# Optimization experiments

Hardware: AMD Instinct MI355X
Metric: run time of the kernel (lower is better)

## Reference

```python
import jax, jax.numpy as jnp
import numpy as np

EPS = 1e-6
B, N, I, H, O, L = 8, 2048, 64, 128, 8, 3
K = O * L
ITERS, TAU, LAM, KNN = 3, 0.1, 0.5, 5

def _ln(x, g, b):
    m = x.mean(-1, keepdims=True)
    v = jnp.mean((x - m) ** 2, -1, keepdims=True)
    return (x - m) / jnp.sqrt(v + 1e-5) * g + b

def _gelu(x):
    return jax.nn.gelu(x, approximate=False)


def setup_inputs():
    ks = jax.random.split(jax.random.key(0), 16)
    rn = lambda k, sh, s=0.05: jax.random.normal(k, sh, jnp.float32) * s
    return {
        'x': jax.random.normal(ks[0], (B, N, I), jnp.float32),
        'enc_w1': rn(ks[1], (H, I)), 'enc_b1': jnp.zeros((H,), jnp.float32),
        'enc_g1': jnp.ones((H,), jnp.float32), 'enc_bb1': jnp.zeros((H,), jnp.float32),
        'enc_w2': rn(ks[2], (H, H)), 'enc_b2': jnp.zeros((H,), jnp.float32),
        'enc_g2': jnp.ones((H,), jnp.float32), 'enc_bb2': jnp.zeros((H,), jnp.float32),
        'sp_w1': rn(ks[3], (H, H + 1)), 'sp_b1': jnp.zeros((H,), jnp.float32),
        'sp_g': jnp.ones((H,), jnp.float32), 'sp_bb': jnp.zeros((H,), jnp.float32),
        'sp_w2': rn(ks[4], (1, H), 0.005), 'sp_b2': jnp.zeros((1,), jnp.float32),
        'object_space': rn(ks[5], (1, O, H), 0.1),
        'horizon_scale': jnp.float32(0.3),
        'level_times': jnp.array([1.0, 2.5, 4.0], jnp.float32),
        'base_horizons': jnp.array([0.9, 0.6, 0.3], jnp.float32),
        'gru_w_ih': rn(ks[6], (3 * H, H)), 'gru_w_hh': rn(ks[7], (3 * H, H)),
        'gru_b_ih': jnp.zeros((3 * H,), jnp.float32), 'gru_b_hh': jnp.zeros((3 * H,), jnp.float32),
        'mlp_w1': rn(ks[8], (H, H)), 'mlp_b1': jnp.zeros((H,), jnp.float32),
        'mlp_w2': rn(ks[9], (H, H)), 'mlp_b2': jnp.zeros((H,), jnp.float32),
        'norm_g': jnp.ones((H,), jnp.float32), 'norm_b': jnp.zeros((H,), jnp.float32),
    }


def reference(x, enc_w1, enc_b1, enc_g1, enc_bb1, enc_w2, enc_b2, enc_g2, enc_bb2, sp_w1, sp_b1, sp_g, sp_bb, sp_w2, sp_b2, object_space, horizon_scale, level_times, base_horizons, gru_w_ih, gru_w_hh, gru_b_ih, gru_b_hh, mlp_w1, mlp_b1, mlp_w2, mlp_b2, norm_g, norm_b):
    # feature encoder: Linear -> LN -> GELU -> Linear -> LN
    h = _gelu(_ln(x @ enc_w1.T + enc_b1, enc_g1, enc_bb1))
    spatial = _ln(h @ enc_w2.T + enc_b2, enc_g2, enc_bb2)  # (B,N,H)
    # local density via kNN mean distance (torch.cdist equivalent)
    sq = jnp.sum(x * x, -1)
    d2 = sq[:, :, None] + sq[:, None, :] - 2.0 * jnp.einsum('bnd,bmd->bnm', x, x)
    dist = jnp.sqrt(jnp.maximum(d2, 0.0))
    knn = -jax.lax.top_k(-dist, KNN + 1)[0]           # k+1 smallest, ascending
    density = jnp.tanh(knn[..., 1:].mean(-1))          # (B,N)
    # scale predictor: Linear -> LN -> GELU -> Linear -> Softplus
    s = jnp.concatenate([spatial, density[..., None]], -1)
    s = _gelu(_ln(s @ sp_w1.T + sp_b1, sp_g, sp_bb))
    pred_scale = jax.nn.softplus(s @ sp_w2.T + sp_b2)  # (B,N,1)
    pred_time = 5.0 - 1.5 * density[..., None] + 0.5 * pred_scale
    features = jnp.concatenate([pred_time, spatial], -1)  # (B,N,H+1)
    # scale-adaptive horizons, tiled object-major to match slot layout
    hz = jnp.clip(base_horizons[None, :, None] + (horizon_scale * (density - 0.5))[:, None, :], 0.1, 1.0)
    horizons = jnp.tile(hz, (1, O, 1))                 # (B,K,N)
    # worldlines
    obj = jnp.broadcast_to(object_space, (B, O, H))
    times = jnp.broadcast_to(jnp.tile(level_times, O)[None, :, None], (B, K, 1))
    slots = jnp.concatenate([times, jnp.repeat(obj, L, axis=1)], -1)  # (B,K,H+1)
    feats_sp = features[..., 1:]
    old_flat = obj.reshape(-1, H)
    attn = None
    for _ in range(ITERS):
        diff = features[:, None, :, :] - slots[:, :, None, :]  # (B,K,N,H+1)
        dt = diff[..., 0]
        dr2 = jnp.sum(diff[..., 1:] ** 2, -1)
        ls = dt * dt - dr2
        d_L = jnp.sign(ls) * jnp.sqrt(jnp.abs(ls) + EPS)
        r = jnp.sqrt(dr2)
        cone = horizons - r / (jnp.abs(dt) + EPS) - 10.0 * jax.nn.relu(-dt) - 5.0 * jax.nn.relu(r - jnp.abs(dt))
        logits = -jnp.abs(d_L) + LAM * jnp.tanh(cone)
        attn = jax.nn.softmax(logits / TAU, axis=1)      # softmax over slots
        w = attn / (attn.sum(2, keepdims=True) + 1e-8)
        upd = jnp.einsum('bkn,bnh->bkh', w, feats_sp)
        obj_upd = upd.reshape(B, O, L, H).sum(2).reshape(-1, H)
        # GRUCell (torch semantics)
        gi = obj_upd @ gru_w_ih.T + gru_b_ih
        gh = old_flat @ gru_w_hh.T + gru_b_hh
        gi_r, gi_z, gi_n = jnp.split(gi, 3, -1)
        gh_r, gh_z, gh_n = jnp.split(gh, 3, -1)
        rg = jax.nn.sigmoid(gi_r + gh_r)
        zg = jax.nn.sigmoid(gi_z + gh_z)
        ng = jnp.tanh(gi_n + rg * gh_n)
        new = ((1.0 - zg) * ng + zg * old_flat).reshape(B, O, H)
        t = _gelu(_ln(new, norm_g, norm_b) @ mlp_w1.T + mlp_b1) @ mlp_w2.T + mlp_b2
        new = new + 0.2 * t
        slots = jnp.concatenate([times, jnp.repeat(new, L, axis=1)], -1)
    return slots, attn, pred_time[..., 0], density
```

## Files before the change

### kernel.cpp

```cpp
#include <hip/hip_runtime.h>
#include <math.h>

constexpr int cB = 8, cN = 2048, cI = 64, cH = 128, cO = 8, cK = 24;
constexpr int ROWS = cB * cN;

constexpr size_t WS_SPATIAL = 0;
constexpr size_t WS_SQ      = WS_SPATIAL + (size_t)ROWS * cH;
constexpr size_t WS_GHS     = WS_SQ + ROWS;
constexpr size_t WS_NSQ0    = WS_GHS + (size_t)cO * 3 * cH;
constexpr size_t WS_NEWOBJ  = WS_NSQ0 + cO;
constexpr size_t WS_NSQ     = WS_NEWOBJ + (size_t)cB * cO * cH;
constexpr size_t WS_W1T     = WS_NSQ + (size_t)cB * cO;
constexpr size_t WS_W2T     = WS_W1T + 8192;
constexpr size_t WS_HW1T    = WS_W2T + 16384;
constexpr size_t WS_UPD3    = WS_HW1T + 16896;
constexpr size_t WS_S3      = WS_UPD3 + (size_t)3 * cB * cK * cH;
constexpr size_t WS_XBF     = WS_S3 + (size_t)3 * cB * cK;

constexpr size_t OUT_SLOTS = 0;
constexpr size_t OUT_ATTN  = (size_t)cB * cK * 129;
constexpr size_t OUT_PT    = OUT_ATTN + (size_t)cB * cK * cN;
constexpr size_t OUT_DEN   = OUT_PT + (size_t)cB * cN;

typedef __attribute__((ext_vector_type(8))) short bf16x8;
typedef __attribute__((ext_vector_type(4))) float f32x4;

__device__ __forceinline__ float gelu_f(float v){
  return 0.5f * v * (1.f + erff(v * 0.70710678118654752440f));
}
__device__ __forceinline__ short f2bf(float f){
  unsigned u = __float_as_uint(f);
  u += 0x7fffu + ((u >> 16) & 1u);
  return (short)(u >> 16);
}
__device__ __forceinline__ bf16x8 pack8(float4 a, float4 b){
  bf16x8 r;
  r[0]=f2bf(a.x); r[1]=f2bf(a.y); r[2]=f2bf(a.z); r[3]=f2bf(a.w);
  r[4]=f2bf(b.x); r[5]=f2bf(b.y); r[6]=f2bf(b.z); r[7]=f2bf(b.w);
  return r;
}
__device__ __forceinline__ float wred(float a){
  a += __shfl_xor(a, 1); a += __shfl_xor(a, 2); a += __shfl_xor(a, 4);
  a += __shfl_xor(a, 8); a += __shfl_xor(a, 16); a += __shfl_xor(a, 32);
  return a;
}

__global__ __launch_bounds__(256) void k_cvt_sq(const float* __restrict__ x, short* __restrict__ xbf,
                                                float* __restrict__ sq){
  int t = threadIdx.x;
  size_t base = (size_t)blockIdx.x * 2048;
  int r = t >> 3, e0 = (t & 7) * 8;
  const float4* xp = (const float4*)(x + base + (size_t)r * cI + e0);
  float4 v0 = xp[0], v1 = xp[1];
  *(bf16x8*)(xbf + base + (size_t)r * cI + e0) = pack8(v0, v1);
  float s = v0.x*v0.x + v0.y*v0.y + v0.z*v0.z + v0.w*v0.w
          + v1.x*v1.x + v1.y*v1.y + v1.z*v1.z + v1.w*v1.w;
  s += __shfl_xor(s, 1); s += __shfl_xor(s, 2); s += __shfl_xor(s, 4);
  if ((t & 7) == 0) sq[blockIdx.x * 32 + r] = s;
}

__global__ __launch_bounds__(256) void k_prep(const float* __restrict__ objsp, const float* __restrict__ w_hh,
                                              const float* __restrict__ b_hh,
                                              const float* __restrict__ ew1, const float* __restrict__ ew2,
                                              const float* __restrict__ spw1,
                                              float* __restrict__ ghs, float* __restrict__ nsq0,
                                              float* __restrict__ w1t, float* __restrict__ w2t,
                                              float* __restrict__ hw1t){
  int id = blockIdx.x * 256 + threadIdx.x;
  if (id < cO * 3 * cH){
    int o = id / (3 * cH), j = id % (3 * cH);
    const float* wr = w_hh + (size_t)j * cH;
    const float* ob = objsp + (size_t)o * cH;
    float a0=0,a1=0,a2=0,a3=0;
    #pragma unroll
    for (int h = 0; h < cH; h += 4){
      a0 += wr[h]*ob[h]; a1 += wr[h+1]*ob[h+1]; a2 += wr[h+2]*ob[h+2]; a3 += wr[h+3]*ob[h+3];
    }
    ghs[id] = (a0+a1)+(a2+a3) + b_hh[j];
  } else if (id < cO * 3 * cH + cO){
    int o = id - cO * 3 * cH;
    const float* ob = objsp + (size_t)o * cH;
    float s = 0.f;
    for (int h = 0; h < cH; ++h) s += ob[h]*ob[h];
    nsq0[o] = s;
  } else {
    int idx = id - (cO * 3 * cH + cO);
    if (idx < 8192){
      int dc = idx >> 9, rem = idx & 511, f = rem >> 2, j = rem & 3;
      w1t[idx] = ew1[f * cI + dc * 4 + j];
    } else if (idx < 24576){
      int k2 = idx - 8192;
      int dc = k2 >> 9, rem = k2 & 511, f = rem >> 2, j = rem & 3;
      w2t[k2] = ew2[f * cH + dc * 4 + j];
    } else if (idx < 41472){
      int k3 = idx - 24576;
      int dc = k3 >> 9, rem = k3 & 511, f = rem >> 2, j = rem & 3;
      int d = dc * 4 + j;
      hw1t[k3] = (d < 129) ? spw1[f * 129 + d] : 0.f;
    }
  }
}

__global__ __launch_bounds__(256) void k_pairwise(const short* __restrict__ xbf, const float* __restrict__ sq,
                                                  float* __restrict__ den_out){
  __shared__ float cand[4][16][101];
  int b  = blockIdx.x >> 7;
  int rt = blockIdx.x & 127;
  int r0 = rt * 16;
  int lane = threadIdx.x & 63, w = threadIdx.x >> 6;
  const short* xb = xbf + (size_t)b * cN * cI;

  int arow = r0 + (lane & 15);
  int koff = (lane >> 4) * 8;
  const bf16x8* ap = (const bf16x8*)(xb + (size_t)arow * cI + koff);
  bf16x8 a0 = ap[0];
  bf16x8 a1 = ap[4];

  float sqr[4];
  int rg0 = r0 + ((lane >> 4) << 2);
  #pragma unroll
  for (int j = 0; j < 4; ++j) sqr[j] = sq[b * cN + rg0 + j];

  float t6[4][6];
  #pragma unroll
  for (int j = 0; j < 4; ++j){
    #pragma unroll
    for (int q = 0; q < 6; ++q) t6[j][q] = 3e38f;
  }

  int cbase = w * 512;
  #pragma unroll 2
  for (int ct = 0; ct < 32; ++ct){
    int col0 = cbase + ct * 16;
    int brow = col0 + (lane & 15);
    const bf16x8* bp = (const bf16x8*)(xb + (size_t)brow * cI + koff);
    bf16x8 b0 = bp[0];
    bf16x8 b1 = bp[4];
    f32x4 acc = {0.f, 0.f, 0.f, 0.f};
    acc = __builtin_amdgcn_mfma_f32_16x16x32_bf16(a0, b0, acc, 0, 0, 0);
    acc = __builtin_amdgcn_mfma_f32_16x16x32_bf16(a1, b1, acc, 0, 0, 0);
    float sqc = sq[b * cN + col0 + (lane & 15)];
    #pragma unroll
    for (int j = 0; j < 4; ++j){
      float d2 = sqr[j] + sqc - 2.f * acc[j];
      d2 = fmaxf(d2, 0.f);
      if (d2 < t6[j][5]){
        if (d2 < t6[j][4]){ t6[j][5]=t6[j][4];
          if (d2 < t6[j][3]){ t6[j][4]=t6[j][3];
            if (d2 < t6[j][2]){ t6[j][3]=t6[j][2];
              if (d2 < t6[j][1]){ t6[j][2]=t6[j][1];
                if (d2 < t6[j][0]){ t6[j][1]=t6[j][0]; t6[j][0]=d2; } else t6[j][1]=d2;
              } else t6[j][2]=d2;
            } else t6[j][3]=d2;
          } else t6[j][4]=d2;
        } else t6[j][5]=d2;
      }
    }
  }
  int rloc = (lane >> 4) << 2;
  #pragma unroll
  for (int j = 0; j < 4; ++j){
    #pragma unroll
    for (int q = 0; q < 6; ++q) cand[w][rloc + j][(lane & 15) * 6 + q] = t6[j][q];
  }
  __syncthreads();
  int tt = threadIdx.x;
  if (tt < 64){
    int ww = tt >> 4, rr = tt & 15;
    const float* c = cand[ww][rr];
    float m0=3e38f,m1=3e38f,m2=3e38f,m3=3e38f,m4=3e38f,m5=3e38f;
    #pragma unroll
    for (int q = 0; q < 96; ++q){
      float v = c[q];
      if (v < m5){
        if (v<m4){ m5=m4; if (v<m3){ m4=m3; if (v<m2){ m3=m2; if (v<m1){ m2=m1; if (v<m0){ m1=m0; m0=v; } else m1=v; } else m2=v; } else m3=v; } else m4=v; } else m5=v;
      }
    }
    float* cw = cand[ww][rr];
    cw[0]=m0; cw[1]=m1; cw[2]=m2; cw[3]=m3; cw[4]=m4; cw[5]=m5;
  }
  __syncthreads();
  if (tt < 16){
    float m0=3e38f,m1=3e38f,m2=3e38f,m3=3e38f,m4=3e38f,m5=3e38f;
    #pragma unroll
    for (int ww = 0; ww < 4; ++ww){
      const float* c = cand[ww][tt];
      #pragma unroll
      for (int q = 0; q < 6; ++q){
        float v = c[q];
        if (v < m5){
          if (v<m4){ m5=m4; if (v<m3){ m4=m3; if (v<m2){ m3=m2; if (v<m1){ m2=m1; if (v<m0){ m1=m0; m0=v; } else m1=v; } else m2=v; } else m3=v; } else m4=v; } else m5=v;
        }
      }
    }
    float md = (sqrtf(m1)+sqrtf(m2)+sqrtf(m3)+sqrtf(m4)+sqrtf(m5)) * 0.2f;
    den_out[b * cN + r0 + tt] = tanhf(md);
  }
}

__global__ __launch_bounds__(256) void k_enc_head(const float* __restrict__ x, const float* __restrict__ den_in,
    const float* __restrict__ w1t, const float* __restrict__ b1v, const float* __restrict__ g1, const float* __restrict__ bb1,
    const float* __restrict__ w2t, const float* __restrict__ b2v, const float* __restrict__ g2, const float* __restrict__ bb2,
    const float* __restrict__ hw1t, const float* __restrict__ hb1, const float* __restrict__ hg, const float* __restrict__ hbb,
    const float* __restrict__ hw2, const float* __restrict__ hb2,
    float* __restrict__ spatial, float* __restrict__ pt_out){
  __shared__ __align__(16) float xbuf[32][68];
  __shared__ __align__(16) float hbuf[32][132];
  const int t = threadIdx.x, lane = t & 63, wid = t >> 6;
  const int row0 = blockIdx.x * 32;
  const int rbase = wid * 8;
  const int f0 = lane * 2;

  {
    const float4* xs = (const float4*)(x + (size_t)row0 * cI);
    #pragma unroll
    for (int i = 0; i < 2; ++i){
      int idx = t + i * 256;
      float4 v = xs[idx];
      *(float4*)&xbuf[idx >> 4][(idx & 15) * 4] = v;
    }
  }
  if (lane < 8){
    float dn = den_in[row0 + rbase + lane];
    float* hd = &hbuf[rbase + lane][128];
    hd[0] = dn; hd[1] = 0.f; hd[2] = 0.f; hd[3] = 0.f;
  }
  __syncthreads();

  float2 b1p  = *(const float2*)(b1v + f0);
  float2 g1p  = *(const float2*)(g1  + f0);
  float2 bb1p = *(const float2*)(bb1 + f0);
  float2 b2p  = *(const float2*)(b2v + f0);
  float2 g2p  = *(const float2*)(g2  + f0);
  float2 bb2p = *(const float2*)(bb2 + f0);
  float2 hb1p = *(const float2*)(hb1 + f0);
  float2 hgp  = *(const float2*)(hg  + f0);
  float2 hbbp = *(const float2*)(hbb + f0);
  float2 hw2p = *(const float2*)(hw2 + f0);

  float accA[8], accB[8];

  #pragma unroll
  for (int r = 0; r < 8; ++r){ accA[r] = b1p.x; accB[r] = b1p.y; }
  #pragma unroll 2
  for (int dc = 0; dc < 16; ++dc){
    float4 wA = *(const float4*)(w1t + ((size_t)dc * cH + f0) * 4);
    float4 wB = *(const float4*)(w1t + ((size_t)dc * cH + f0 + 1) * 4);
    #pragma unroll
    for (int r = 0; r < 8; ++r){
      float4 xv = *(const float4*)&xbuf[rbase + r][dc * 4];
      accA[r] += wA.x*xv.x + wA.y*xv.y + wA.z*xv.z + wA.w*xv.w;
      accB[r] += wB.x*xv.x + wB.y*xv.y + wB.z*xv.z + wB.w*xv.w;
    }
  }
  #pragma unroll
  for (int r = 0; r < 8; ++r){
    float sm = wred(accA[r] + accB[r]);
    float s2 = wred(accA[r]*accA[r] + accB[r]*accB[r]);
    float mean = sm * (1.f/128.f);
    float rstd = rsqrtf(s2 * (1.f/128.f) - mean*mean + 1e-5f);
    float hA = gelu_f((accA[r]-mean)*rstd*g1p.x + bb1p.x);
    float hB = gelu_f((accB[r]-mean)*rstd*g1p.y + bb1p.y);
    float2 hv = { hA, hB };
    *(float2*)&hbuf[rbase + r][f0] = hv;
  }
  __syncthreads();

  #pragma unroll
  for (int r = 0; r < 8; ++r){ accA[r] = b2p.x; accB[r] = b2p.y; }
  #pragma unroll 2
  for (int dc = 0; dc < 32; ++dc){
    float4 wA = *(const float4*)(w2t + ((size_t)dc * cH + f0) * 4);
    float4 wB = *(const float4*)(w2t + ((size_t)dc * cH + f0 + 1) * 4);
    #pragma unroll
    for (int r = 0; r < 8; ++r){
      float4 hv = *(const float4*)&hbuf[rbase + r][dc * 4];
      accA[r] += wA.x*hv.x + wA.y*hv.y + wA.z*hv.z + wA.w*hv.w;
      accB[r] += wB.x*hv.x + wB.y*hv.y + wB.z*hv.z + wB.w*hv.w;
    }
  }
  #pragma unroll
  for (int r = 0; r < 8; ++r){
    float sm = wred(accA[r] + accB[r]);
    float s2 = wred(accA[r]*accA[r] + accB[r]*accB[r]);
    float mean = sm * (1.f/128.f);
    float rstd = rsqrtf(s2 * (1.f/128.f) - mean*mean + 1e-5f);
    float sA = (accA[r]-mean)*rstd*g2p.x + bb2p.x;
    float sB = (accB[r]-mean)*rstd*g2p.y + bb2p.y;
    float2 sv = { sA, sB };
    *(float2*)(spatial + (size_t)(row0 + rbase + r) * cH + f0) = sv;
    *(float2*)&hbuf[rbase + r][f0] = sv;
  }
  __syncthreads();

  #pragma unroll
  for (int r = 0; r < 8; ++r){ accA[r] = hb1p.x; accB[r] = hb1p.y; }
  #pragma unroll 2
  for (int dc = 0; dc < 33; ++dc){
    float4 wA = *(const float4*)(hw1t + ((size_t)dc * cH + f0) * 4);
    float4 wB = *(const float4*)(hw1t + ((size_t)dc * cH + f0 + 1) * 4);
    #pragma unroll
    for (int r = 0; r < 8; ++r){
      float4 hv = *(const float4*)&hbuf[rbase + r][dc * 4];
      accA[r] += wA.x*hv.x + wA.y*hv.y + wA.z*hv.z + wA.w*hv.w;
      accB[r] += wB.x*hv.x + wB.y*hv.y + wB.z*hv.z + wB.w*hv.w;
    }
  }
  #pragma unroll
  for (int r = 0; r < 8; ++r){
    float sm = wred(accA[r] + accB[r]);
    float s2 = wred(accA[r]*accA[r] + accB[r]*accB[r]);
    float mean = sm * (1.f/128.f);
    float rstd = rsqrtf(s2 * (1.f/128.f) - mean*mean + 1e-5f);
    float e0 = gelu_f((accA[r]-mean)*rstd*hgp.x + hbbp.x);
    float e1 = gelu_f((accB[r]-mean)*rstd*hgp.y + hbbp.y);
    float part = wred(e0*hw2p.x + e1*hw2p.y);
    if (lane == r){
      float ps = part + hb2[0];
      float spl = fmaxf(ps, 0.f) + log1pf(expf(-fabsf(ps)));
      float dn = hbuf[rbase + r][128];
      pt_out[row0 + rbase + r] = 5.f - 1.5f*dn + 0.5f*spl;
    }
  }
}

__global__ __launch_bounds__(256) void k_attn(const float* __restrict__ spatial, const float* __restrict__ pt_in,
    const float* __restrict__ den_in, const float* __restrict__ objp, int ob_stride,
    const float* __restrict__ nsqp, int nq_stride,
    const float* __restrict__ lt, const float* __restrict__ bh, const float* __restrict__ hs,
    float* __restrict__ attn_out){
  int t = threadIdx.x;
  int sub = t & 3, rl = t >> 2;
  int id = blockIdx.x * 64 + rl;
  int b = id >> 11, n = id & 2047;

  float4 sv[8];
  const float4* sp4 = (const float4*)(spatial + (size_t)id * cH + sub * 32);
  #pragma unroll
  for (int i = 0; i < 8; ++i) sv[i] = sp4[i];
  float spn2 = 0.f;
  #pragma unroll
  for (int i = 0; i < 8; ++i) spn2 += sv[i].x*sv[i].x + sv[i].y*sv[i].y + sv[i].z*sv[i].z + sv[i].w*sv[i].w;

  const float* ob = objp + (size_t)b * ob_stride;
  float acc[8];
  #pragma unroll
  for (int o = 0; o < 8; ++o){
    const float4* orow = (const float4*)(ob + (size_t)o * cH + sub * 32);
    float a0=0,a1=0,a2=0,a3=0;
    #pragma unroll
    for (int i = 0; i < 8; ++i){ float4 w4 = orow[i];
      a0 += w4.x*sv[i].x; a1 += w4.y*sv[i].y; a2 += w4.z*sv[i].z; a3 += w4.w*sv[i].w; }
    acc[o] = (a0+a1)+(a2+a3);
  }
  spn2 += __shfl_xor(spn2, 1); spn2 += __shfl_xor(spn2, 2);
  #pragma unroll
  for (int o = 0; o < 8; ++o){ acc[o] += __shfl_xor(acc[o], 1); acc[o] += __shfl_xor(acc[o], 2); }

  if (sub != 0) return;

  const float* nq = nsqp + (size_t)b * nq_stride;
  float nsqv_[8];
  #pragma unroll
  for (int o = 0; o < 8; ++o) nsqv_[o] = nq[o];
  float pt = pt_in[id], den = den_in[id];
  float hsv = hs[0];
  float lts[3] = { lt[0], lt[1], lt[2] };
  float bhs[3] = { bh[0], bh[1], bh[2] };

  float logits[24];
  #pragma unroll
  for (int k = 0; k < 24; ++k){
    const int o = k / 3, l = k % 3;
    float dtv = pt - lts[l];
    float dr2 = fmaxf(spn2 + nsqv_[o] - 2.f * acc[o], 0.f);
    float ls  = dtv*dtv - dr2;
    float adL = sqrtf(fabsf(ls) + 1e-6f);
    float r   = sqrtf(dr2);
    float adt = fabsf(dtv);
    float hz  = fminf(fmaxf(bhs[l] + hsv * (den - 0.5f), 0.1f), 1.0f);
    float cone = hz - r / (adt + 1e-6f) - 10.f * fmaxf(-dtv, 0.f) - 5.f * fmaxf(r - adt, 0.f);
    logits[k] = (-adL + 0.5f * tanhf(cone)) * 10.f;
  }
  float mx = -3e38f;
  #pragma unroll
  for (int k = 0; k < 24; ++k) mx = fmaxf(mx, logits[k]);
  float es[24]; float ssum = 0.f;
  #pragma unroll
  for (int k = 0; k < 24; ++k){ es[k] = expf(logits[k] - mx); ssum += es[k]; }
  float inv = 1.f / ssum;
  float* ao = attn_out + (size_t)b * cK * cN + n;
  #pragma unroll
  for (int k = 0; k < 24; ++k) ao[(size_t)k * cN] = es[k] * inv;
}

__global__ __launch_bounds__(256) void k_upd(const float* __restrict__ spatial, const float* __restrict__ attn,
                                             float* __restrict__ upd_raw, float* __restrict__ Ssum){
  __shared__ float abuf[24][64];
  int blk = blockIdx.x;
  int b = blk >> 5, chunk = blk & 31;
  int n0 = chunk * 64;
  int t = threadIdx.x;
  const float* ab = attn + (size_t)b * cK * cN + n0;
  #pragma unroll
  for (int i = 0; i < 6; ++i){
    int idx = t + i * 256;
    abuf[idx >> 6][idx & 63] = ab[(size_t)(idx >> 6) * cN + (idx & 63)];
  }
  __syncthreads();
  int h = t & 127, g = t >> 7;
  float acc[12];
  #pragma unroll
  for (int kk = 0; kk < 12; ++kk) acc[kk] = 0.f;
  const float* sp = spatial + ((size_t)b * cN + n0) * cH + h;
  for (int ni = 0; ni < 64; ++ni){
    float spv = sp[(size_t)ni * cH];
    #pragma unroll
    for (int kk = 0; kk < 12; ++kk) acc[kk] += abuf[g*12+kk][ni] * spv;
  }
  #pragma unroll
  for (int kk = 0; kk < 12; ++kk)
    atomicAdd(&upd_raw[((size_t)b * cK + g*12+kk) * cH + h], acc[kk]);
  if (t < 24){
    float s = 0.f;
    #pragma unroll
    for (int j = 0; j < 64; ++j) s += abuf[t][j];
    atomicAdd(&Ssum[b * cK + t], s);
  }
}

__global__ __launch_bounds__(128) void k_gru(const float* __restrict__ upd_raw, const float* __restrict__ Ssum,
    const float* __restrict__ ghs, const float* __restrict__ objsp,
    const float* __restrict__ w_ih, const float* __restrict__ b_ih,
    const float* __restrict__ mw1, const float* __restrict__ mb1,
    const float* __restrict__ mw2, const float* __restrict__ mb2,
    const float* __restrict__ ng_, const float* __restrict__ nb_,
    const float* __restrict__ lt,
    float* __restrict__ newobj, float* __restrict__ nsq,
    float* __restrict__ slots_out, int writeSlots){
  __shared__ float ubuf[cH], lbuf[cH], gbuf[cH], red[8];
  int bo = blockIdx.x; int b = bo >> 3, o = bo & 7;
  int t = threadIdx.x;
  int lane = t & 63, wid = t >> 6;

  float u = 0.f;
  #pragma unroll
  for (int l = 0; l < 3; ++l){
    int k = o * 3 + l;
    float s = Ssum[b * cK + k] + 1e-8f;
    u += upd_raw[((size_t)b * cK + k) * cH + t] / s;
  }
  ubuf[t] = u;
  __syncthreads();

  float gi[3];
  #pragma unroll
  for (int j3 = 0; j3 < 3; ++j3){
    const float* wr = w_ih + ((size_t)j3 * cH + t) * cH;
    float a0=0,a1=0,a2=0,a3=0;
    #pragma unroll
    for (int d = 0; d < cH; d += 4){
      a0 += wr[d]*ubuf[d]; a1 += wr[d+1]*ubuf[d+1]; a2 += wr[d+2]*ubuf[d+2]; a3 += wr[d+3]*ubuf[d+3];
    }
    gi[j3] = (a0+a1)+(a2+a3) + b_ih[j3 * cH + t];
  }
  const float* gh = ghs + (size_t)o * 3 * cH;
  float ghr = gh[t], ghz = gh[cH + t], ghn = gh[2 * cH + t];
  float oldv = objsp[(size_t)o * cH + t];
  float rg = 1.f / (1.f + expf(-(gi[0] + ghr)));
  float zg = 1.f / (1.f + expf(-(gi[1] + ghz)));
  float ngv = tanhf(gi[2] + rg * ghn);
  float nv = (1.f - zg) * ngv + zg * oldv;

  float s1 = nv, s2 = nv * nv;
  #pragma unroll
  for (int m = 1; m < 64; m <<= 1){ s1 += __shfl_xor(s1, m); s2 += __shfl_xor(s2, m); }
  if (lane == 0){ red[wid] = s1; red[4 + wid] = s2; }
  __syncthreads();
  float mean = (red[0] + red[1]) * (1.f/128.f);
  float var  = (red[4] + red[5]) * (1.f/128.f) - mean * mean;
  float ln = (nv - mean) * rsqrtf(var + 1e-5f) * ng_[t] + nb_[t];
  lbuf[t] = ln;
  __syncthreads();

  const float* w1r = mw1 + (size_t)t * cH;
  {
    float a0=0,a1=0,a2=0,a3=0;
    #pragma unroll
    for (int d = 0; d < cH; d += 4){
      a0 += w1r[d]*lbuf[d]; a1 += w1r[d+1]*lbuf[d+1]; a2 += w1r[d+2]*lbuf[d+2]; a3 += w1r[d+3]*lbuf[d+3];
    }
    gbuf[t] = gelu_f((a0+a1)+(a2+a3) + mb1[t]);
  }
  __syncthreads();
  const float* w2r = mw2 + (size_t)t * cH;
  float m2v;
  {
    float a0=0,a1=0,a2=0,a3=0;
    #pragma unroll
    for (int d = 0; d < cH; d += 4){
      a0 += w2r[d]*gbuf[d]; a1 += w2r[d+1]*gbuf[d+1]; a2 += w2r[d+2]*gbuf[d+2]; a3 += w2r[d+3]*gbuf[d+3];
    }
    m2v = (a0+a1)+(a2+a3) + mb2[t];
  }
  float outv = nv + 0.2f * m2v;
  newobj[((size_t)b * cO + o) * cH + t] = outv;

  float qv = outv * outv;
  #pragma unroll
  for (int m = 1; m < 64; m <<= 1) qv += __shfl_xor(qv, m);
  __syncthreads();
  if (lane == 0) red[wid] = qv;
  __syncthreads();
  if (t == 0) nsq[b * cO + o] = red[0] + red[1];

  if (writeSlots){
    #pragma unroll
    for (int l = 0; l < 3; ++l){
      size_t base = ((size_t)b * cK + o * 3 + l) * 129;
      slots_out[base + 1 + t] = outv;
      if (t == 0) slots_out[base] = lt[l];
    }
  }
}

extern "C" void kernel_launch(void* const* d_in, const int* in_sizes, int n_in,
                              void* d_out, int out_size, void* d_ws, size_t ws_size,
                              hipStream_t stream){
  const float* x       = (const float*)d_in[0];
  const float* enc_w1  = (const float*)d_in[1];
  const float* enc_b1  = (const float*)d_in[2];
  const float* enc_g1  = (const float*)d_in[3];
  const float* enc_bb1 = (const float*)d_in[4];
  const float* enc_w2  = (const float*)d_in[5];
  const float* enc_b2  = (const float*)d_in[6];
  const float* enc_g2  = (const float*)d_in[7];
  const float* enc_bb2 = (const float*)d_in[8];
  const float* sp_w1   = (const float*)d_in[9];
  const float* sp_b1   = (const float*)d_in[10];
  const float* sp_g    = (const float*)d_in[11];
  const float* sp_bb   = (const float*)d_in[12];
  const float* sp_w2   = (const float*)d_in[13];
  const float* sp_b2   = (const float*)d_in[14];
  const float* objsp   = (const float*)d_in[15];
  const float* hscale  = (const float*)d_in[16];
  const float* ltimes  = (const float*)d_in[17];
  const float* bhor    = (const float*)d_in[18];
  const float* gw_ih   = (const float*)d_in[19];
  const float* gw_hh   = (const float*)d_in[20];
  const float* gb_ih   = (const float*)d_in[21];
  const float* gb_hh   = (const float*)d_in[22];
  const float* mw1     = (const float*)d_in[23];
  const float* mb1     = (const float*)d_in[24];
  const float* mw2     = (const float*)d_in[25];
  const float* mb2     = (const float*)d_in[26];
  const float* normg   = (const float*)d_in[27];
  const float* normb   = (const float*)d_in[28];
  (void)in_sizes; (void)n_in; (void)out_size; (void)ws_size;

  float* out = (float*)d_out;
  float* ws  = (float*)d_ws;

  float* spatial = ws + WS_SPATIAL;
  float* sq      = ws + WS_SQ;
  float* ghs     = ws + WS_GHS;
  float* nsq0    = ws + WS_NSQ0;
  float* newobj  = ws + WS_NEWOBJ;
  float* nsqv    = ws + WS_NSQ;
  float* w1t     = ws + WS_W1T;
  float* w2t     = ws + WS_W2T;
  float* hw1t    = ws + WS_HW1T;
  float* updr3   = ws + WS_UPD3;
  float* Ss3     = ws + WS_S3;
  short* xbf     = (short*)(ws + WS_XBF);

  hipMemsetAsync((void*)updr3, 0, (size_t)(3 * cB * cK * cH + 3 * cB * cK) * sizeof(float), stream);

  k_cvt_sq<<<dim3(ROWS / 32), dim3(256), 0, stream>>>(x, xbf, sq);
  k_prep<<<dim3(175), dim3(256), 0, stream>>>(objsp, gw_hh, gb_hh, enc_w1, enc_w2, sp_w1,
                                              ghs, nsq0, w1t, w2t, hw1t);
  k_pairwise<<<dim3(cB * (cN / 16)), dim3(256), 0, stream>>>(xbf, sq, out + OUT_DEN);
  k_enc_head<<<dim3(ROWS / 32), dim3(256), 0, stream>>>(x, out + OUT_DEN,
      w1t, enc_b1, enc_g1, enc_bb1, w2t, enc_b2, enc_g2, enc_bb2,
      hw1t, sp_b1, sp_g, sp_bb, sp_w2, sp_b2,
      spatial, out + OUT_PT);

  for (int it = 0; it < 3; ++it){
    float* updr = updr3 + (size_t)it * cB * cK * cH;
    float* Ss   = Ss3 + (size_t)it * cB * cK;
    const float* objp = (it == 0) ? objsp : newobj;
    int obst = (it == 0) ? 0 : cO * cH;
    const float* nqp = (it == 0) ? nsq0 : nsqv;
    int nqst = (it == 0) ? 0 : cO;
    k_attn<<<dim3(ROWS / 64), dim3(256), 0, stream>>>(spatial, out + OUT_PT, out + OUT_DEN,
                                                      objp, obst, nqp, nqst,
                                                      ltimes, bhor, hscale, out + OUT_ATTN);
    k_upd<<<dim3(cB * 32), dim3(256), 0, stream>>>(spatial, out + OUT_ATTN, updr, Ss);
    k_gru<<<dim3(cB * cO), dim3(128), 0, stream>>>(updr, Ss, ghs, objsp, gw_ih, gb_ih,
                                                   mw1, mb1, mw2, mb2, normg, normb, ltimes,
                                                   newobj, nsqv, out + OUT_SLOTS, (it == 2) ? 1 : 0);
  }
}
```

Baseline: 339.9 us.

## Fuse attention softmax into update kernel and halve encoder rows per block

Merges the attention-logit/softmax kernel with the weighted-update reduction, so attention probabilities stay in shared memory instead of going through global memory. The attention output is now written only on the last iteration, which cuts global writes and one launch per iteration. The encoder/head kernel is also reworked to process 16 rows per block instead of 32, doubling the grid and raising the unroll factor, which trades weight reuse for more parallelism. Writing attention only on the final iteration is valid because earlier iterations' attention is overwritten anyway.

```diff
diff --git a/kernel.cpp b/kernel.cpp
--- a/kernel.cpp
+++ b/kernel.cpp
@@ -204,25 +204,21 @@
     const float* __restrict__ hw1t, const float* __restrict__ hb1, const float* __restrict__ hg, const float* __restrict__ hbb,
     const float* __restrict__ hw2, const float* __restrict__ hb2,
     float* __restrict__ spatial, float* __restrict__ pt_out){
-  __shared__ __align__(16) float xbuf[32][68];
-  __shared__ __align__(16) float hbuf[32][132];
+  __shared__ __align__(16) float xbuf[16][68];
+  __shared__ __align__(16) float hbuf[16][132];
   const int t = threadIdx.x, lane = t & 63, wid = t >> 6;
-  const int row0 = blockIdx.x * 32;
-  const int rbase = wid * 8;
+  const int row0 = blockIdx.x * 16;
+  const int rbase = wid * 4;
   const int f0 = lane * 2;
 
   {
     const float4* xs = (const float4*)(x + (size_t)row0 * cI);
-    #pragma unroll
-    for (int i = 0; i < 2; ++i){
-      int idx = t + i * 256;
-      float4 v = xs[idx];
-      *(float4*)&xbuf[idx >> 4][(idx & 15) * 4] = v;
-    }
-  }
-  if (lane < 8){
-    float dn = den_in[row0 + rbase + lane];
-    float* hd = &hbuf[rbase + lane][128];
+    float4 v = xs[t];
+    *(float4*)&xbuf[t >> 4][(t & 15) * 4] = v;
+  }
+  if (t < 16){
+    float dn = den_in[row0 + t];
+    float* hd = &hbuf[t][128];
     hd[0] = dn; hd[1] = 0.f; hd[2] = 0.f; hd[3] = 0.f;
   }
   __syncthreads();
@@ -238,23 +234,23 @@
   float2 hbbp = *(const float2*)(hbb + f0);
   float2 hw2p = *(const float2*)(hw2 + f0);
 
-  float accA[8], accB[8];
-
-  #pragma unroll
-  for (int r = 0; r < 8; ++r){ accA[r] = b1p.x; accB[r] = b1p.y; }
-  #pragma unroll 2
+  float accA[4], accB[4];
+
+  #pragma unroll
+  for (int r = 0; r < 4; ++r){ accA[r] = b1p.x; accB[r] = b1p.y; }
+  #pragma unroll 4
   for (int dc = 0; dc < 16; ++dc){
     float4 wA = *(const float4*)(w1t + ((size_t)dc * cH + f0) * 4);
     float4 wB = *(const float4*)(w1t + ((size_t)dc * cH + f0 + 1) * 4);
     #pragma unroll
-    for (int r = 0; r < 8; ++r){
+    for (int r = 0; r < 4; ++r){
       float4 xv = *(const float4*)&xbuf[rbase + r][dc * 4];
       accA[r] += wA.x*xv.x + wA.y*xv.y + wA.z*xv.z + wA.w*xv.w;
       accB[r] += wB.x*xv.x + wB.y*xv.y + wB.z*xv.z + wB.w*xv.w;
     }
   }
   #pragma unroll
-  for (int r = 0; r < 8; ++r){
+  for (int r = 0; r < 4; ++r){
     float sm = wred(accA[r] + accB[r]);
     float s2 = wred(accA[r]*accA[r] + accB[r]*accB[r]);
     float mean = sm * (1.f/128.f);
@@ -267,20 +263,20 @@
   __syncthreads();
 
   #pragma unroll
-  for (int r = 0; r < 8; ++r){ accA[r] = b2p.x; accB[r] = b2p.y; }
-  #pragma unroll 2
+  for (int r = 0; r < 4; ++r){ accA[r] = b2p.x; accB[r] = b2p.y; }
+  #pragma unroll 4
   for (int dc = 0; dc < 32; ++dc){
     float4 wA = *(const float4*)(w2t + ((size_t)dc * cH + f0) * 4);
     float4 wB = *(const float4*)(w2t + ((size_t)dc * cH + f0 + 1) * 4);
     #pragma unroll
-    for (int r = 0; r < 8; ++r){
+    for (int r = 0; r < 4; ++r){
       float4 hv = *(const float4*)&hbuf[rbase + r][dc * 4];
       accA[r] += wA.x*hv.x + wA.y*hv.y + wA.z*hv.z + wA.w*hv.w;
       accB[r] += wB.x*hv.x + wB.y*hv.y + wB.z*hv.z + wB.w*hv.w;
     }
   }
   #pragma unroll
-  for (int r = 0; r < 8; ++r){
+  for (int r = 0; r < 4; ++r){
     float sm = wred(accA[r] + accB[r]);
     float s2 = wred(accA[r]*accA[r] + accB[r]*accB[r]);
     float mean = sm * (1.f/128.f);
@@ -294,20 +290,20 @@
   __syncthreads();
 
   #pragma unroll
-  for (int r = 0; r < 8; ++r){ accA[r] = hb1p.x; accB[r] = hb1p.y; }
-  #pragma unroll 2
+  for (int r = 0; r < 4; ++r){ accA[r] = hb1p.x; accB[r] = hb1p.y; }
+  #pragma unroll 4
   for (int dc = 0; dc < 33; ++dc){
     float4 wA = *(const float4*)(hw1t + ((size_t)dc * cH + f0) * 4);
     float4 wB = *(const float4*)(hw1t + ((size_t)dc * cH + f0 + 1) * 4);
     #pragma unroll
-    for (int r = 0; r < 8; ++r){
+    for (int r = 0; r < 4; ++r){
       float4 hv = *(const float4*)&hbuf[rbase + r][dc * 4];
       accA[r] += wA.x*hv.x + wA.y*hv.y + wA.z*hv.z + wA.w*hv.w;
       accB[r] += wB.x*hv.x + wB.y*hv.y + wB.z*hv.z + wB.w*hv.w;
     }
   }
   #pragma unroll
-  for (int r = 0; r < 8; ++r){
+  for (int r = 0; r < 4; ++r){
     float sm = wred(accA[r] + accB[r]);
     float s2 = wred(accA[r]*accA[r] + accB[r]*accB[r]);
     float mean = sm * (1.f/128.f);
@@ -324,103 +320,103 @@
   }
 }
 
-__global__ __launch_bounds__(256) void k_attn(const float* __restrict__ spatial, const float* __restrict__ pt_in,
+__global__ __launch_bounds__(256) void k_attn_upd(const float* __restrict__ spatial, const float* __restrict__ pt_in,
     const float* __restrict__ den_in, const float* __restrict__ objp, int ob_stride,
     const float* __restrict__ nsqp, int nq_stride,
     const float* __restrict__ lt, const float* __restrict__ bh, const float* __restrict__ hs,
-    float* __restrict__ attn_out){
-  int t = threadIdx.x;
-  int sub = t & 3, rl = t >> 2;
-  int id = blockIdx.x * 64 + rl;
-  int b = id >> 11, n = id & 2047;
-
-  float4 sv[8];
-  const float4* sp4 = (const float4*)(spatial + (size_t)id * cH + sub * 32);
-  #pragma unroll
-  for (int i = 0; i < 8; ++i) sv[i] = sp4[i];
-  float spn2 = 0.f;
-  #pragma unroll
-  for (int i = 0; i < 8; ++i) spn2 += sv[i].x*sv[i].x + sv[i].y*sv[i].y + sv[i].z*sv[i].z + sv[i].w*sv[i].w;
-
-  const float* ob = objp + (size_t)b * ob_stride;
-  float acc[8];
-  #pragma unroll
-  for (int o = 0; o < 8; ++o){
-    const float4* orow = (const float4*)(ob + (size_t)o * cH + sub * 32);
-    float a0=0,a1=0,a2=0,a3=0;
-    #pragma unroll
-    for (int i = 0; i < 8; ++i){ float4 w4 = orow[i];
-      a0 += w4.x*sv[i].x; a1 += w4.y*sv[i].y; a2 += w4.z*sv[i].z; a3 += w4.w*sv[i].w; }
-    acc[o] = (a0+a1)+(a2+a3);
-  }
-  spn2 += __shfl_xor(spn2, 1); spn2 += __shfl_xor(spn2, 2);
-  #pragma unroll
-  for (int o = 0; o < 8; ++o){ acc[o] += __shfl_xor(acc[o], 1); acc[o] += __shfl_xor(acc[o], 2); }
-
-  if (sub != 0) return;
-
-  const float* nq = nsqp + (size_t)b * nq_stride;
-  float nsqv_[8];
-  #pragma unroll
-  for (int o = 0; o < 8; ++o) nsqv_[o] = nq[o];
-  float pt = pt_in[id], den = den_in[id];
-  float hsv = hs[0];
-  float lts[3] = { lt[0], lt[1], lt[2] };
-  float bhs[3] = { bh[0], bh[1], bh[2] };
-
-  float logits[24];
-  #pragma unroll
-  for (int k = 0; k < 24; ++k){
-    const int o = k / 3, l = k % 3;
-    float dtv = pt - lts[l];
-    float dr2 = fmaxf(spn2 + nsqv_[o] - 2.f * acc[o], 0.f);
-    float ls  = dtv*dtv - dr2;
-    float adL = sqrtf(fabsf(ls) + 1e-6f);
-    float r   = sqrtf(dr2);
-    float adt = fabsf(dtv);
-    float hz  = fminf(fmaxf(bhs[l] + hsv * (den - 0.5f), 0.1f), 1.0f);
-    float cone = hz - r / (adt + 1e-6f) - 10.f * fmaxf(-dtv, 0.f) - 5.f * fmaxf(r - adt, 0.f);
-    logits[k] = (-adL + 0.5f * tanhf(cone)) * 10.f;
-  }
-  float mx = -3e38f;
-  #pragma unroll
-  for (int k = 0; k < 24; ++k) mx = fmaxf(mx, logits[k]);
-  float es[24]; float ssum = 0.f;
-  #pragma unroll
-  for (int k = 0; k < 24; ++k){ es[k] = expf(logits[k] - mx); ssum += es[k]; }
-  float inv = 1.f / ssum;
-  float* ao = attn_out + (size_t)b * cK * cN + n;
-  #pragma unroll
-  for (int k = 0; k < 24; ++k) ao[(size_t)k * cN] = es[k] * inv;
-}
-
-__global__ __launch_bounds__(256) void k_upd(const float* __restrict__ spatial, const float* __restrict__ attn,
-                                             float* __restrict__ upd_raw, float* __restrict__ Ssum){
-  __shared__ float abuf[24][64];
+    float* __restrict__ attn_out, int writeAttn,
+    float* __restrict__ upd_raw, float* __restrict__ Ssum){
+  __shared__ float abuf[24][65];
   int blk = blockIdx.x;
   int b = blk >> 5, chunk = blk & 31;
   int n0 = chunk * 64;
   int t = threadIdx.x;
-  const float* ab = attn + (size_t)b * cK * cN + n0;
-  #pragma unroll
-  for (int i = 0; i < 6; ++i){
-    int idx = t + i * 256;
-    abuf[idx >> 6][idx & 63] = ab[(size_t)(idx >> 6) * cN + (idx & 63)];
-  }
-  __syncthreads();
+  int sub = t & 3, rl = t >> 2;
+  int id = b * cN + n0 + rl;
+
+  {
+    float4 sv[8];
+    const float4* sp4 = (const float4*)(spatial + (size_t)id * cH + sub * 32);
+    #pragma unroll
+    for (int i = 0; i < 8; ++i) sv[i] = sp4[i];
+    float spn2 = 0.f;
+    #pragma unroll
+    for (int i = 0; i < 8; ++i) spn2 += sv[i].x*sv[i].x + sv[i].y*sv[i].y + sv[i].z*sv[i].z + sv[i].w*sv[i].w;
+
+    const float* ob = objp + (size_t)b * ob_stride;
+    float acc[8];
+    #pragma unroll
+    for (int o = 0; o < 8; ++o){
+      const float4* orow = (const float4*)(ob + (size_t)o * cH + sub * 32);
+      float a0=0,a1=0,a2=0,a3=0;
+      #pragma unroll
+      for (int i = 0; i < 8; ++i){ float4 w4 = orow[i];
+        a0 += w4.x*sv[i].x; a1 += w4.y*sv[i].y; a2 += w4.z*sv[i].z; a3 += w4.w*sv[i].w; }
+      acc[o] = (a0+a1)+(a2+a3);
+    }
+    spn2 += __shfl_xor(spn2, 1); spn2 += __shfl_xor(spn2, 2);
+    #pragma unroll
+    for (int o = 0; o < 8; ++o){ acc[o] += __shfl_xor(acc[o], 1); acc[o] += __shfl_xor(acc[o], 2); }
+
+    if (sub == 0){
+      const float* nq = nsqp + (size_t)b * nq_stride;
+      float nsqv_[8];
+      #pragma unroll
+      for (int o = 0; o < 8; ++o) nsqv_[o] = nq[o];
+      float pt = pt_in[id], den = den_in[id];
+      float hsv = hs[0];
+      float lts[3] = { lt[0], lt[1], lt[2] };
+      float bhs[3] = { bh[0], bh[1], bh[2] };
+
+      float logits[24];
+      #pragma unroll
+      for (int k = 0; k < 24; ++k){
+        const int o = k / 3, l = k % 3;
+        float dtv = pt - lts[l];
+        float dr2 = fmaxf(spn2 + nsqv_[o] - 2.f * acc[o], 0.f);
+        float ls  = dtv*dtv - dr2;
+        float adL = sqrtf(fabsf(ls) + 1e-6f);
+        float r   = sqrtf(dr2);
+        float adt = fabsf(dtv);
+        float hz  = fminf(fmaxf(bhs[l] + hsv * (den - 0.5f), 0.1f), 1.0f);
+        float cone = hz - r / (adt + 1e-6f) - 10.f * fmaxf(-dtv, 0.f) - 5.f * fmaxf(r - adt, 0.f);
+        logits[k] = (-adL + 0.5f * tanhf(cone)) * 10.f;
+      }
+      float mx = -3e38f;
+      #pragma unroll
+      for (int k = 0; k < 24; ++k) mx = fmaxf(mx, logits[k]);
+      float es[24]; float ssum = 0.f;
+      #pragma unroll
+      for (int k = 0; k < 24; ++k){ es[k] = expf(logits[k] - mx); ssum += es[k]; }
+      float inv = 1.f / ssum;
+      #pragma unroll
+      for (int k = 0; k < 24; ++k) abuf[k][rl] = es[k] * inv;
+    }
+  }
+  __syncthreads();
+
+  if (writeAttn){
+    float* ao = attn_out + (size_t)b * cK * cN + n0;
+    #pragma unroll
+    for (int i = 0; i < 6; ++i){
+      int idx = t + i * 256;
+      ao[(size_t)(idx >> 6) * cN + (idx & 63)] = abuf[idx >> 6][idx & 63];
+    }
+  }
+
   int h = t & 127, g = t >> 7;
-  float acc[12];
-  #pragma unroll
-  for (int kk = 0; kk < 12; ++kk) acc[kk] = 0.f;
+  float acc2[12];
+  #pragma unroll
+  for (int kk = 0; kk < 12; ++kk) acc2[kk] = 0.f;
   const float* sp = spatial + ((size_t)b * cN + n0) * cH + h;
   for (int ni = 0; ni < 64; ++ni){
     float spv = sp[(size_t)ni * cH];
     #pragma unroll
-    for (int kk = 0; kk < 12; ++kk) acc[kk] += abuf[g*12+kk][ni] * spv;
+    for (int kk = 0; kk < 12; ++kk) acc2[kk] += abuf[g*12+kk][ni] * spv;
   }
   #pragma unroll
   for (int kk = 0; kk < 12; ++kk)
-    atomicAdd(&upd_raw[((size_t)b * cK + g*12+kk) * cH + h], acc[kk]);
+    atomicAdd(&upd_raw[((size_t)b * cK + g*12+kk) * cH + h], acc2[kk]);
   if (t < 24){
     float s = 0.f;
     #pragma unroll
@@ -580,7 +576,7 @@
   k_prep<<<dim3(175), dim3(256), 0, stream>>>(objsp, gw_hh, gb_hh, enc_w1, enc_w2, sp_w1,
                                               ghs, nsq0, w1t, w2t, hw1t);
   k_pairwise<<<dim3(cB * (cN / 16)), dim3(256), 0, stream>>>(xbf, sq, out + OUT_DEN);
-  k_enc_head<<<dim3(ROWS / 32), dim3(256), 0, stream>>>(x, out + OUT_DEN,
+  k_enc_head<<<dim3(ROWS / 16), dim3(256), 0, stream>>>(x, out + OUT_DEN,
       w1t, enc_b1, enc_g1, enc_bb1, w2t, enc_b2, enc_g2, enc_bb2,
       hw1t, sp_b1, sp_g, sp_bb, sp_w2, sp_b2,
       spatial, out + OUT_PT);
@@ -592,10 +588,11 @@
     int obst = (it == 0) ? 0 : cO * cH;
     const float* nqp = (it == 0) ? nsq0 : nsqv;
     int nqst = (it == 0) ? 0 : cO;
-    k_attn<<<dim3(ROWS / 64), dim3(256), 0, stream>>>(spatial, out + OUT_PT, out + OUT_DEN,
-                                                      objp, obst, nqp, nqst,
-                                                      ltimes, bhor, hscale, out + OUT_ATTN);
-    k_upd<<<dim3(cB * 32), dim3(256), 0, stream>>>(spatial, out + OUT_ATTN, updr, Ss);
+    k_attn_upd<<<dim3(cB * 32), dim3(256), 0, stream>>>(spatial, out + OUT_PT, out + OUT_DEN,
+                                                        objp, obst, nqp, nqst,
+                                                        ltimes, bhor, hscale,
+                                                        out + OUT_ATTN, (it == 2) ? 1 : 0,
+                                                        updr, Ss);
     k_gru<<<dim3(cB * cO), dim3(128), 0, stream>>>(updr, Ss, ghs, objsp, gw_ih, gb_ih,
                                                    mw1, mb1, mw2, mb2, normg, normb, ltimes,
                                                    newobj, nsqv, out + OUT_SLOTS, (it == 2) ? 1 : 0);
```

Result: no change. 340.5 us (+0.2%).
